# Optimization experiments

Hardware: AMD Instinct MI355X
Metric: run time of the kernel (lower is better)

## Reference

```python
import jax, jax.numpy as jnp
import numpy as np
import math

B, L, D, P = 2, 2048, 256, 32
PI = math.pi


def _layernorm(x, g, b, eps=1e-5):
    m = x.mean(-1, keepdims=True)
    v = x.var(-1, keepdims=True)
    return (x - m) / jnp.sqrt(v + eps) * g + b


def setup_inputs() -> dict:
    key = jax.random.key(0)
    ks = jax.random.split(key, 16)
    sd = 1.0 / math.sqrt(D)
    f32 = jnp.float32
    inp = {
        "x": jax.random.normal(ks[0], (B, L, D), f32),
        # key_encoder: Linear(D, P)
        "key_W": jax.random.normal(ks[1], (D, P), f32) * sd,
        "key_b": jnp.zeros((P,), f32),
        # value_encoder: Linear(D, D)
        "val_W": jax.random.normal(ks[2], (D, D), f32) * sd,
        "val_b": jnp.zeros((D,), f32),
        # refiner: LayerNorm(D), Linear(D, 2D), GELU, Linear(2D, D)
        "ln1_g": jnp.ones((D,), f32),
        "ln1_b": jnp.zeros((D,), f32),
        "W1": jax.random.normal(ks[3], (D, 2 * D), f32) * sd,
        "b1": jnp.zeros((2 * D,), f32),
        "W2": jax.random.normal(ks[4], (2 * D, D), f32) * (1.0 / math.sqrt(2 * D)),
        "b2": jnp.zeros((D,), f32),
        # to_out: LayerNorm(D), Linear(D, D)
        "ln2_g": jnp.ones((D,), f32),
        "ln2_b": jnp.zeros((D,), f32),
        "Wo": jax.random.normal(ks[5], (D, D), f32) * sd,
        "bo": jnp.zeros((D,), f32),
    }
    return inp


def reference(x, key_W, key_b, val_W, val_b, ln1_g, ln1_b, W1, b1, W2, b2,
              ln2_g, ln2_b, Wo, bo):
    # key phases in (-pi, pi); phasor exp(i*theta) handled as (cos, sin)
    phases = jnp.tanh(x @ key_W + key_b) * PI          # (B, L, P)
    values = x @ val_W + val_b                          # (B, L, D)

    cos_p = jnp.cos(phases)
    sin_p = jnp.sin(phases)
    # torch.roll(shifts=1, dims=1) then zero the first position -> shift right, row 0 = 0
    zrow = jnp.zeros_like(cos_p[:, :1])
    cos_s = jnp.concatenate([zrow, cos_p[:, :-1]], axis=1)
    sin_s = jnp.concatenate([zrow, sin_p[:, :-1]], axis=1)

    # odd positions hold values
    vmask = (jnp.arange(L) % 2 == 1).astype(x.dtype)    # (L,)
    mv = values * vmask[None, :, None]                  # (B, L, D)

    # bind: outer product phasor (P) x value (D); real/imag parts
    bound_re = cos_s[..., None] * mv[:, :, None, :]     # (B, L, P, D)
    bound_im = sin_s[..., None] * mv[:, :, None, :]
    mem_re = jnp.cumsum(bound_re, axis=1)
    mem_im = jnp.cumsum(bound_im, axis=1)

    # retrieve: Re[ memory * exp(-i*theta) ] summed over phases
    retrieved = (jnp.einsum('blpd,blp->bld', mem_re, cos_p)
                 + jnp.einsum('blpd,blp->bld', mem_im, sin_p))

    valid = jnp.maximum(jnp.cumsum(vmask), 1.0)         # (L,)
    retrieved = retrieved / (jnp.sqrt(valid)[None, :, None] * math.sqrt(P))

    h = _layernorm(retrieved, ln1_g, ln1_b)
    h = jax.nn.gelu(h @ W1 + b1, approximate=False)
    refined = h @ W2 + b2
    out = x + (_layernorm(refined, ln2_g, ln2_b) @ Wo + bo)
    return out
```

## Files before the change

### kernel.cpp

```cpp
#include <hip/hip_runtime.h>
#include <math.h>

#define BB 2
#define LL 2048
#define DD 256
#define PP 32
#define NC 64
#define PI_F 3.14159265358979323846f

typedef __attribute__((ext_vector_type(8))) short bf16x8;
typedef __attribute__((ext_vector_type(4))) float f32x4;
typedef unsigned short ushort_t;
typedef unsigned int uint_t;

__device__ inline ushort_t f2bf(float x) {
    uint_t u = __float_as_uint(x);
    uint_t r = (u + 0x7fffu + ((u >> 16) & 1u)) >> 16;
    return (ushort_t)r;
}

__global__ __launch_bounds__(256) void prep_key_kernel(
    const float* __restrict__ W1, const float* __restrict__ W2,
    const float* __restrict__ Wo, const float* __restrict__ valW,
    const float* __restrict__ x, const float* __restrict__ key_W,
    const float* __restrict__ key_b,
    ushort_t* __restrict__ W1t, ushort_t* __restrict__ W2t,
    ushort_t* __restrict__ Wot, ushort_t* __restrict__ valWt,
    float2* __restrict__ ph)
{
    const int bid = blockIdx.x;
    const int t = threadIdx.x;
    if (bid < 96) {
        __shared__ float T[64][65];
        const float* W; ushort_t* Wt; int K, N, tile;
        if (bid < 32)      { W = W1;   Wt = W1t;   K = 256; N = 512; tile = bid; }
        else if (bid < 64) { W = W2;   Wt = W2t;   K = 512; N = 256; tile = bid - 32; }
        else if (bid < 80) { W = Wo;   Wt = Wot;   K = 256; N = 256; tile = bid - 64; }
        else               { W = valW; Wt = valWt; K = 256; N = 256; tile = bid - 80; }
        const int ntiles = N / 64;
        const int k0 = (tile / ntiles) * 64, n0 = (tile % ntiles) * 64;
        {
            const int rr = t >> 2, cb = (t & 3) * 16;
            #pragma unroll
            for (int i = 0; i < 16; i += 4) {
                const float4 v = *(const float4*)&W[(k0 + rr) * N + n0 + cb + i];
                T[rr][cb + i + 0] = v.x; T[rr][cb + i + 1] = v.y;
                T[rr][cb + i + 2] = v.z; T[rr][cb + i + 3] = v.w;
            }
        }
        __syncthreads();
        {
            const int n = t >> 2, kb = (t & 3) * 16;
            #pragma unroll
            for (int i = 0; i < 16; ++i)
                Wt[(n0 + n) * K + k0 + kb + i] = f2bf(T[kb + i][n]);
        }
    } else {
        __shared__ ushort_t xt[16][264];
        __shared__ ushort_t kwT[32][264];
        __shared__ float rbuf[4][2][16][17];
        const int row0 = (bid - 96) * 16;
        {
            const int l = t >> 4, cb = (t & 15) * 16;
            const float* src = &x[(long)(row0 + l) * DD + cb];
            ushort_t tmp[16];
            #pragma unroll
            for (int i = 0; i < 4; ++i) {
                const float4 v = *(const float4*)&src[i * 4];
                tmp[i*4+0] = f2bf(v.x); tmp[i*4+1] = f2bf(v.y);
                tmp[i*4+2] = f2bf(v.z); tmp[i*4+3] = f2bf(v.w);
            }
            *(uint4*)&xt[l][cb]     = *(uint4*)&tmp[0];
            *(uint4*)&xt[l][cb + 8] = *(uint4*)&tmp[8];
        }
        {
            #pragma unroll
            for (int i = 0; i < 8; ++i) {
                const int idx4 = i * 256 + t;
                const int k = idx4 >> 3, pc = (idx4 & 7) * 4;
                const float4 v = *(const float4*)&key_W[k * 32 + pc];
                kwT[pc + 0][k] = f2bf(v.x);
                kwT[pc + 1][k] = f2bf(v.y);
                kwT[pc + 2][k] = f2bf(v.z);
                kwT[pc + 3][k] = f2bf(v.w);
            }
        }
        __syncthreads();
        const int wv = t >> 6, lane = t & 63;
        const int qd = lane >> 4, mc = lane & 15;
        f32x4 acc0 = {0.f,0.f,0.f,0.f}, acc1 = {0.f,0.f,0.f,0.f};
        #pragma unroll
        for (int ks = 0; ks < 2; ++ks) {
            const int ko = wv * 64 + ks * 32 + qd * 8;
            const bf16x8 a  = *(const bf16x8*)&xt[mc][ko];
            const bf16x8 b0 = *(const bf16x8*)&kwT[mc][ko];
            const bf16x8 b1 = *(const bf16x8*)&kwT[16 + mc][ko];
            acc0 = __builtin_amdgcn_mfma_f32_16x16x32_bf16(a, b0, acc0, 0, 0, 0);
            acc1 = __builtin_amdgcn_mfma_f32_16x16x32_bf16(a, b1, acc1, 0, 0, 0);
        }
        #pragma unroll
        for (int r = 0; r < 4; ++r) {
            rbuf[wv][0][qd * 4 + r][mc] = acc0[r];
            rbuf[wv][1][qd * 4 + r][mc] = acc1[r];
        }
        __syncthreads();
        #pragma unroll
        for (int rep = 0; rep < 2; ++rep) {
            const int idx = rep * 256 + t;
            const int p = idx & 31, l = idx >> 5;
            const int nf = p >> 4, mcol = p & 15;
            float a = key_b[p] + rbuf[0][nf][l][mcol] + rbuf[1][nf][l][mcol]
                    + rbuf[2][nf][l][mcol] + rbuf[3][nf][l][mcol];
            a = tanhf(a) * PI_F;
            float sn, cs;
            sincosf(a, &sn, &cs);
            ph[(long)(row0 + l) * PP + p] = make_float2(cs, sn);
        }
    }
}

__global__ __launch_bounds__(256) void valbind_kernel(
    const float* __restrict__ x, const float2* __restrict__ ph,
    const ushort_t* __restrict__ valWt, const float* __restrict__ val_b,
    ushort_t* __restrict__ VoddT, float* __restrict__ Mt)
{
    __shared__ ushort_t xsb[16][264];
    __shared__ ushort_t VdT[64][40];
    __shared__ ushort_t phsT[64][40];
    __shared__ float    Ms[64][68];

    const int tid = threadIdx.x;
    const int bid = blockIdx.x;
    const int b  = bid >> 8;
    const int c  = (bid >> 2) & 63;
    const int dq = bid & 3;
    const int base = b * LL;
    const int r0 = 32 * c;

    {
        const int j = tid >> 4, cb = (tid & 15) * 16;
        const float* src = &x[(long)(base + r0 + 2 * j + 1) * DD + cb];
        ushort_t tmp[16];
        #pragma unroll
        for (int i = 0; i < 4; ++i) {
            const float4 v = *(const float4*)&src[i * 4];
            tmp[i*4+0] = f2bf(v.x); tmp[i*4+1] = f2bf(v.y);
            tmp[i*4+2] = f2bf(v.z); tmp[i*4+3] = f2bf(v.w);
        }
        *(uint4*)&xsb[j][cb]     = *(uint4*)&tmp[0];
        *(uint4*)&xsb[j][cb + 8] = *(uint4*)&tmp[8];
    }
    {
        const int j = tid >> 4, qb = (tid & 15) * 4;
        const float4 v = *(const float4*)((const float*)ph +
                              (long)(base + r0 + 2 * j) * 64 + qb);
        phsT[qb + 0][j] = f2bf(v.x);
        phsT[qb + 1][j] = f2bf(v.y);
        phsT[qb + 2][j] = f2bf(v.z);
        phsT[qb + 3][j] = f2bf(v.w);
    }
    for (int e = tid; e < 64 * 16; e += 256) {
        phsT[e >> 4][16 + (e & 15)] = 0;
        VdT[e >> 4][16 + (e & 15)] = 0;
    }
    __syncthreads();

    const int wv = tid >> 6, lane = tid & 63;
    const int qd = lane >> 4, mc = lane & 15;

    f32x4 va = {0.f,0.f,0.f,0.f};
    const int dloc = wv * 16 + mc;
    const int ng = dq * 64 + dloc;
    const ushort_t* B0 = &valWt[(long)ng * 256];
    #pragma unroll
    for (int ks = 0; ks < 8; ++ks) {
        const bf16x8 a  = *(const bf16x8*)&xsb[mc][ks * 32 + qd * 8];
        const bf16x8 b0 = *(const bf16x8*)&B0[ks * 32 + qd * 8];
        va = __builtin_amdgcn_mfma_f32_16x16x32_bf16(a, b0, va, 0, 0, 0);
    }
    {
        const float bb = val_b[ng];
        #pragma unroll
        for (int r = 0; r < 4; ++r)
            VdT[dloc][qd * 4 + r] = f2bf(va[r] + bb);
    }
    __syncthreads();

    const bf16x8 a2 = *(const bf16x8*)&phsT[wv * 16 + mc][qd * 8];
    f32x4 macc[4];
    #pragma unroll
    for (int nf = 0; nf < 4; ++nf) {
        f32x4 z = {0.f,0.f,0.f,0.f};
        const bf16x8 b2 = *(const bf16x8*)&VdT[nf * 16 + mc][qd * 8];
        macc[nf] = __builtin_amdgcn_mfma_f32_16x16x32_bf16(a2, b2, z, 0, 0, 0);
    }
    #pragma unroll
    for (int nf = 0; nf < 4; ++nf) {
        #pragma unroll
        for (int r = 0; r < 4; ++r)
            Ms[nf * 16 + mc][wv * 16 + qd * 4 + r] = macc[nf][r];
    }
    __syncthreads();

    {
        float* dst = &Mt[((long)(b * NC + c) * 256 + dq * 64) * 64];
        #pragma unroll
        for (int p = 0; p < 4; ++p) {
            const int idx4 = p * 256 + tid;
            const int dl = idx4 >> 4, q4 = (idx4 & 15) * 4;
            *(float4*)&dst[dl * 64 + q4] = *(const float4*)&Ms[dl][q4];
        }
    }
    if (tid < 64) {
        ushort_t* vd = &VoddT[((long)(b * NC + c) * 256 + dq * 64 + tid) * 16];
        *(uint4*)&vd[0] = *(const uint4*)&VdT[tid][0];
        *(uint4*)&vd[8] = *(const uint4*)&VdT[tid][8];
    }
}

__global__ __launch_bounds__(256) void prefix_kernel(
    const float* __restrict__ M, ushort_t* __restrict__ Mpre_b)
{
    __shared__ float segsum[4][64];
    const int tid = threadIdx.x;
    const int b  = blockIdx.x >> 8;
    const int cg = blockIdx.x & 255;
    const int col = cg * 64 + (tid & 63);
    const int seg = tid >> 6;
    const long base = (long)b * NC * 16384 + col;

    float v[16], s = 0.f;
    #pragma unroll
    for (int i = 0; i < 16; ++i) {
        v[i] = M[base + (long)(seg * 16 + i) * 16384];
        s += v[i];
    }
    segsum[seg][tid & 63] = s;
    __syncthreads();
    float run = 0.f;
    #pragma unroll
    for (int sg = 0; sg < 3; ++sg)
        if (sg < seg) run += segsum[sg][tid & 63];
    #pragma unroll
    for (int i = 0; i < 16; ++i) {
        const long a = base + (long)(seg * 16 + i) * 16384;
        Mpre_b[a] = f2bf(run);
        run += v[i];
    }
}

__global__ __launch_bounds__(256) void retrieve_kernel(
    const float* __restrict__ ph, const ushort_t* __restrict__ Mpre_b,
    const ushort_t* __restrict__ VoddT,
    const float* __restrict__ ln1_g, const float* __restrict__ ln1_b,
    ushort_t* __restrict__ rhat)
{
    __shared__ ushort_t Bs_m[256][72];
    __shared__ ushort_t Bs_v[256][32];
    __shared__ ushort_t As_ph[16][72];
    __shared__ ushort_t Bs_sh[16][72];
    __shared__ ushort_t As_p[16][32];
    __shared__ float    ref[16][264];

    const int tid = threadIdx.x;
    const int b = blockIdx.x >> 7;
    const int c = (blockIdx.x >> 1) & 63;
    const int h = blockIdx.x & 1;
    const int l0g = 32 * c + 16 * h;
    const long rowbase = (long)b * LL + l0g;

    {
        const ushort_t* src = &Mpre_b[(long)(b * NC + c) * 16384];
        #pragma unroll
        for (int p = 0; p < 8; ++p) {
            const int idx8 = p * 256 + tid;
            const int d = idx8 >> 3, q8 = (idx8 & 7) * 8;
            *(uint4*)&Bs_m[d][q8] = *(const uint4*)&src[idx8 * 8];
        }
    }
    {
        const int r = tid >> 4, q4 = (tid & 15) * 4;
        const float4 v = *(const float4*)&ph[(rowbase + r) * 64 + q4];
        ushort_t t0[4] = {f2bf(v.x), f2bf(v.y), f2bf(v.z), f2bf(v.w)};
        *(uint2*)&As_ph[r][q4] = *(uint2*)t0;
        const float4 w = *(const float4*)&ph[((long)b * LL + 32 * c + 2 * r) * 64 + q4];
        ushort_t t1[4] = {f2bf(w.x), f2bf(w.y), f2bf(w.z), f2bf(w.w)};
        *(uint2*)&Bs_sh[r][q4] = *(uint2*)t1;
    }
    {
        const ushort_t* src = &VoddT[(long)(b * NC + c) * 4096];
        const int j0 = (tid & 1) * 8;
        *(uint4*)&Bs_v[tid >> 1][j0] = *(const uint4*)&src[tid * 8];
        *(uint4*)&Bs_v[(tid + 256) >> 1][j0] = *(const uint4*)&src[(tid + 256) * 8];
        *(uint4*)&Bs_v[tid][16] = make_uint4(0, 0, 0, 0);
        *(uint4*)&Bs_v[tid][24] = make_uint4(0, 0, 0, 0);
        As_p[tid >> 4][16 + (tid & 15)] = 0;
    }
    __syncthreads();

    const int wv = tid >> 6, lane = tid & 63;
    const int qd = lane >> 4, mc = lane & 15;

    {
        f32x4 sacc = {0.f, 0.f, 0.f, 0.f};
        #pragma unroll
        for (int ks = 0; ks < 2; ++ks) {
            const bf16x8 a  = *(const bf16x8*)&As_ph[mc][ks * 32 + qd * 8];
            const bf16x8 bb = *(const bf16x8*)&Bs_sh[mc][ks * 32 + qd * 8];
            sacc = __builtin_amdgcn_mfma_f32_16x16x32_bf16(a, bb, sacc, 0, 0, 0);
        }
        if (wv == 0) {
            #pragma unroll
            for (int r = 0; r < 4; ++r) {
                const int l = qd * 4 + r;
                As_p[l][mc] = (2 * mc + 1 <= 16 * h + l) ? f2bf(sacc[r])
                                                         : (ushort_t)0;
            }
        }
    }

    f32x4 acc[4];
    #pragma unroll
    for (int i = 0; i < 4; ++i) acc[i] = (f32x4){0.f, 0.f, 0.f, 0.f};
    #pragma unroll
    for (int i = 0; i < 4; ++i) {
        const int d0 = wv * 64 + i * 16;
        #pragma unroll
        for (int ks = 0; ks < 2; ++ks) {
            const bf16x8 a  = *(const bf16x8*)&As_ph[mc][ks * 32 + qd * 8];
            const bf16x8 bb = *(const bf16x8*)&Bs_m[d0 + mc][ks * 32 + qd * 8];
            acc[i] = __builtin_amdgcn_mfma_f32_16x16x32_bf16(a, bb, acc[i], 0, 0, 0);
        }
    }
    __syncthreads();

    {
        const bf16x8 a2 = *(const bf16x8*)&As_p[mc][qd * 8];
        #pragma unroll
        for (int i = 0; i < 4; ++i) {
            const int d0 = wv * 64 + i * 16;
            const bf16x8 b2 = *(const bf16x8*)&Bs_v[d0 + mc][qd * 8];
            acc[i] = __builtin_amdgcn_mfma_f32_16x16x32_bf16(a2, b2, acc[i], 0, 0, 0);
        }
    }

    #pragma unroll
    for (int r = 0; r < 4; ++r) {
        const int l = qd * 4 + r;
        int va = (l0g + l + 1) >> 1; if (va < 1) va = 1;
        const float sc = 0.17677669529663687f * rsqrtf((float)va);
        #pragma unroll
        for (int i = 0; i < 4; ++i)
            ref[l][wv * 64 + i * 16 + mc] = acc[i][r] * sc;
    }
    __syncthreads();

    {
        const int row = tid >> 4, cg = (tid & 15) * 16;
        float s = 0.f, sq = 0.f;
        #pragma unroll
        for (int i = 0; i < 16; ++i) {
            const float v = ref[row][cg + i];
            s += v; sq += v * v;
        }
        s += __shfl_xor(s, 1, 16);  sq += __shfl_xor(sq, 1, 16);
        s += __shfl_xor(s, 2, 16);  sq += __shfl_xor(sq, 2, 16);
        s += __shfl_xor(s, 4, 16);  sq += __shfl_xor(sq, 4, 16);
        s += __shfl_xor(s, 8, 16);  sq += __shfl_xor(sq, 8, 16);
        const float m = s * (1.f / 256.f);
        const float inv = rsqrtf(sq * (1.f / 256.f) - m * m + 1e-5f);
        ushort_t o16[16];
        #pragma unroll
        for (int i = 0; i < 16; ++i) {
            const int cc = cg + i;
            o16[i] = f2bf((ref[row][cc] - m) * inv * ln1_g[cc] + ln1_b[cc]);
        }
        ushort_t* dst = &rhat[(rowbase + row) * DD + cg];
        *(uint4*)&dst[0] = *(uint4*)&o16[0];
        *(uint4*)&dst[8] = *(uint4*)&o16[8];
    }
}

__global__ __launch_bounds__(256) void gemm1_kernel(
    const ushort_t* __restrict__ A, const ushort_t* __restrict__ Bt,
    const float* __restrict__ bias, ushort_t* __restrict__ out)
{
    __shared__ ushort_t As[32][136];
    __shared__ ushort_t Bs[64][136];
    const int tid = threadIdx.x;
    const int mt = blockIdx.x & 127;
    const int nt = blockIdx.x >> 7;
    const int m0 = mt * 32, n0 = nt * 64;
    const int wv = tid >> 6, lane = tid & 63;
    const int qd = lane >> 4, mc = lane & 15;

    f32x4 acc0 = {0.f, 0.f, 0.f, 0.f};
    f32x4 acc1 = {0.f, 0.f, 0.f, 0.f};

    const int ar = tid >> 3, ak = (tid & 7) * 16;
    const int bn = tid >> 2, bk = (tid & 3) * 32;

    for (int k0 = 0; k0 < 256; k0 += 128) {
        __syncthreads();
        {
            const ushort_t* sa = &A[(long)(m0 + ar) * 256 + k0 + ak];
            *(uint4*)&As[ar][ak]     = *(const uint4*)&sa[0];
            *(uint4*)&As[ar][ak + 8] = *(const uint4*)&sa[8];
        }
        {
            const ushort_t* src = &Bt[(long)(n0 + bn) * 256 + k0 + bk];
            *(uint4*)&Bs[bn][bk +  0] = *(const uint4*)&src[0];
            *(uint4*)&Bs[bn][bk +  8] = *(const uint4*)&src[8];
            *(uint4*)&Bs[bn][bk + 16] = *(const uint4*)&src[16];
            *(uint4*)&Bs[bn][bk + 24] = *(const uint4*)&src[24];
        }
        __syncthreads();
        #pragma unroll
        for (int ko = 0; ko < 128; ko += 32) {
            const bf16x8 a0 = *(const bf16x8*)&As[mc][ko + qd * 8];
            const bf16x8 a1 = *(const bf16x8*)&As[16 + mc][ko + qd * 8];
            const bf16x8 b  = *(const bf16x8*)&Bs[wv * 16 + mc][ko + qd * 8];
            acc0 = __builtin_amdgcn_mfma_f32_16x16x32_bf16(a0, b, acc0, 0, 0, 0);
            acc1 = __builtin_amdgcn_mfma_f32_16x16x32_bf16(a1, b, acc1, 0, 0, 0);
        }
    }

    const int nn = n0 + wv * 16 + mc;
    const float bb = bias[nn];
    #pragma unroll
    for (int r = 0; r < 4; ++r) {
        const long row0w = m0 + qd * 4 + r;
        float v0 = acc0[r] + bb;
        float v1 = acc1[r] + bb;
        v0 = 0.5f * v0 * (1.f + erff(v0 * 0.70710678118654752f));
        v1 = 0.5f * v1 * (1.f + erff(v1 * 0.70710678118654752f));
        out[row0w * 512 + nn] = f2bf(v0);
        out[(row0w + 16) * 512 + nn] = f2bf(v1);
    }
}

__global__ __launch_bounds__(256) void gemm23_kernel(
    const ushort_t* __restrict__ h, const ushort_t* __restrict__ W2t,
    const float* __restrict__ b2, const float* __restrict__ ln2_g,
    const float* __restrict__ ln2_b, const ushort_t* __restrict__ Wot,
    const float* __restrict__ bo, const float* __restrict__ x,
    float* __restrict__ out)
{
    __shared__ ushort_t As[16][72];
    __shared__ ushort_t Bs[256][72];
    __shared__ float Ct[16][264];
    __shared__ ushort_t shT[16][264];

    const int tid = threadIdx.x;
    const int m0 = blockIdx.x * 16;
    const int wv = tid >> 6, lane = tid & 63;
    const int qd = lane >> 4, mc = lane & 15;

    f32x4 acc[4];
    #pragma unroll
    for (int nf = 0; nf < 4; ++nf) acc[nf] = (f32x4){0.f,0.f,0.f,0.f};

    const int sr = tid >> 3, sk = (tid & 7) * 8;

    for (int k0 = 0; k0 < 512; k0 += 64) {
        __syncthreads();
        if (tid < 128)
            *(uint4*)&As[sr][sk] = *(const uint4*)&h[(long)(m0 + sr) * 512 + k0 + sk];
        #pragma unroll
        for (int rr = 0; rr < 8; ++rr) {
            const int n = rr * 32 + (tid >> 3);
            *(uint4*)&Bs[n][sk] = *(const uint4*)&W2t[(long)n * 512 + k0 + sk];
        }
        __syncthreads();
        #pragma unroll
        for (int ks = 0; ks < 2; ++ks) {
            const bf16x8 a = *(const bf16x8*)&As[mc][ks * 32 + qd * 8];
            #pragma unroll
            for (int nf = 0; nf < 4; ++nf) {
                const bf16x8 b = *(const bf16x8*)&Bs[wv * 64 + nf * 16 + mc][ks * 32 + qd * 8];
                acc[nf] = __builtin_amdgcn_mfma_f32_16x16x32_bf16(a, b, acc[nf], 0, 0, 0);
            }
        }
    }

    #pragma unroll
    for (int nf = 0; nf < 4; ++nf) {
        const int n = wv * 64 + nf * 16 + mc;
        const float bb = b2[n];
        #pragma unroll
        for (int r = 0; r < 4; ++r)
            Ct[qd * 4 + r][n] = acc[nf][r] + bb;
    }
    __syncthreads();

    {
        const int row = tid >> 4, cg = (tid & 15) * 16;
        float s = 0.f, sq = 0.f;
        #pragma unroll
        for (int i = 0; i < 16; ++i) {
            const float v = Ct[row][cg + i];
            s += v; sq += v * v;
        }
        s  += __shfl_xor(s, 1, 16);  sq += __shfl_xor(sq, 1, 16);
        s  += __shfl_xor(s, 2, 16);  sq += __shfl_xor(sq, 2, 16);
        s  += __shfl_xor(s, 4, 16);  sq += __shfl_xor(sq, 4, 16);
        s  += __shfl_xor(s, 8, 16);  sq += __shfl_xor(sq, 8, 16);
        const float m = s * (1.f / 256.f);
        const float inv = rsqrtf(sq * (1.f / 256.f) - m * m + 1e-5f);
        #pragma unroll
        for (int i = 0; i < 16; ++i) {
            const int cc = cg + i;
            shT[row][cc] = f2bf((Ct[row][cc] - m) * inv * ln2_g[cc] + ln2_b[cc]);
        }
    }

    f32x4 acc2[4];
    #pragma unroll
    for (int nf = 0; nf < 4; ++nf) acc2[nf] = (f32x4){0.f,0.f,0.f,0.f};

    for (int k0 = 0; k0 < 256; k0 += 64) {
        __syncthreads();
        #pragma unroll
        for (int rr = 0; rr < 8; ++rr) {
            const int n = rr * 32 + (tid >> 3);
            *(uint4*)&Bs[n][sk] = *(const uint4*)&Wot[(long)n * 256 + k0 + sk];
        }
        __syncthreads();
        #pragma unroll
        for (int ks = 0; ks < 2; ++ks) {
            const bf16x8 a = *(const bf16x8*)&shT[mc][k0 + ks * 32 + qd * 8];
            #pragma unroll
            for (int nf = 0; nf < 4; ++nf) {
                const bf16x8 b = *(const bf16x8*)&Bs[wv * 64 + nf * 16 + mc][ks * 32 + qd * 8];
                acc2[nf] = __builtin_amdgcn_mfma_f32_16x16x32_bf16(a, b, acc2[nf], 0, 0, 0);
            }
        }
    }

    #pragma unroll
    for (int nf = 0; nf < 4; ++nf) {
        const int n = wv * 64 + nf * 16 + mc;
        const float bb = bo[n];
        #pragma unroll
        for (int r = 0; r < 4; ++r) {
            const long row = m0 + qd * 4 + r;
            out[row * DD + n] = acc2[nf][r] + bb + x[row * DD + n];
        }
    }
}

extern "C" void kernel_launch(void* const* d_in, const int* in_sizes, int n_in,
                              void* d_out, int out_size, void* d_ws, size_t ws_size,
                              hipStream_t stream)
{
    const float* x     = (const float*)d_in[0];
    const float* key_W = (const float*)d_in[1];
    const float* key_b = (const float*)d_in[2];
    const float* val_W = (const float*)d_in[3];
    const float* val_b = (const float*)d_in[4];
    const float* ln1_g = (const float*)d_in[5];
    const float* ln1_b = (const float*)d_in[6];
    const float* W1    = (const float*)d_in[7];
    const float* b1    = (const float*)d_in[8];
    const float* W2    = (const float*)d_in[9];
    const float* b2    = (const float*)d_in[10];
    const float* ln2_g = (const float*)d_in[11];
    const float* ln2_b = (const float*)d_in[12];
    const float* Wo    = (const float*)d_in[13];
    const float* bo    = (const float*)d_in[14];
    float* outp = (float*)d_out;

    float* ws = (float*)d_ws;
    float*  ph      = ws;
    float*  Mt      = ws + 262144;
    ushort_t* Mpre_b = (ushort_t*)(Mt + 2097152);
    ushort_t* VoddT  = Mpre_b + 2097152;
    ushort_t* rhat_b = VoddT + 524288;
    ushort_t* W1t   = rhat_b + 1048576;
    ushort_t* W2t   = W1t + 131072;
    ushort_t* Wot   = W2t + 131072;
    ushort_t* valWt = Wot + 65536;
    ushort_t* h_b    = (ushort_t*)Mt;

    prep_key_kernel<<<352, 256, 0, stream>>>(W1, W2, Wo, val_W, x, key_W, key_b,
                                             W1t, W2t, Wot, valWt, (float2*)ph);
    valbind_kernel<<<512, 256, 0, stream>>>(x, (const float2*)ph, valWt, val_b,
                                            VoddT, Mt);
    prefix_kernel<<<512, 256, 0, stream>>>(Mt, Mpre_b);
    retrieve_kernel<<<256, 256, 0, stream>>>(ph, Mpre_b, VoddT, ln1_g, ln1_b, rhat_b);
    gemm1_kernel<<<1024, 256, 0, stream>>>(rhat_b, W1t, b1, h_b);
    gemm23_kernel<<<256, 256, 0, stream>>>(h_b, W2t, b2, ln2_g, ln2_b,
                                           Wot, bo, x, outp);
}
```

Before: 123.5 us.

## Fuse retrieve, MLP GEMMs and output projection into one kernel

```diff
diff --git a/kernel.cpp b/kernel.cpp
--- a/kernel.cpp
+++ b/kernel.cpp
@@ -249,18 +249,25 @@
     }
 }
 
-__global__ __launch_bounds__(256) void retrieve_kernel(
+__global__ __launch_bounds__(256) void retrieve_mlp_kernel(
     const float* __restrict__ ph, const ushort_t* __restrict__ Mpre_b,
     const ushort_t* __restrict__ VoddT,
     const float* __restrict__ ln1_g, const float* __restrict__ ln1_b,
-    ushort_t* __restrict__ rhat)
+    const ushort_t* __restrict__ W1t, const float* __restrict__ b1,
+    const ushort_t* __restrict__ W2t, const float* __restrict__ b2,
+    const float* __restrict__ ln2_g, const float* __restrict__ ln2_b,
+    const ushort_t* __restrict__ Wot, const float* __restrict__ bo,
+    const float* __restrict__ x, float* __restrict__ out)
 {
     __shared__ ushort_t Bs_m[256][72];
     __shared__ ushort_t Bs_v[256][32];
     __shared__ ushort_t As_ph[16][72];
     __shared__ ushort_t Bs_sh[16][72];
     __shared__ ushort_t As_p[16][32];
-    __shared__ float    ref[16][264];
+    __shared__ float    refct[16][264];
+    __shared__ ushort_t rhat_s[16][264];
+    __shared__ ushort_t h_s[16][520];
+    __shared__ ushort_t shT[16][264];
 
     const int tid = threadIdx.x;
     const int b = blockIdx.x >> 7;
@@ -300,6 +307,7 @@
 
     const int wv = tid >> 6, lane = tid & 63;
     const int qd = lane >> 4, mc = lane & 15;
+    const int sk = (tid & 7) * 8;
 
     {
         f32x4 sacc = {0.f, 0.f, 0.f, 0.f};
@@ -351,7 +359,7 @@
         const float sc = 0.17677669529663687f * rsqrtf((float)va);
         #pragma unroll
         for (int i = 0; i < 4; ++i)
-            ref[l][wv * 64 + i * 16 + mc] = acc[i][r] * sc;
+            refct[l][wv * 64 + i * 16 + mc] = acc[i][r] * sc;
     }
     __syncthreads();
 
@@ -360,7 +368,7 @@
         float s = 0.f, sq = 0.f;
         #pragma unroll
         for (int i = 0; i < 16; ++i) {
-            const float v = ref[row][cg + i];
+            const float v = refct[row][cg + i];
             s += v; sq += v * v;
         }
         s += __shfl_xor(s, 1, 16);  sq += __shfl_xor(sq, 1, 16);
@@ -373,123 +381,77 @@
         #pragma unroll
         for (int i = 0; i < 16; ++i) {
             const int cc = cg + i;
-            o16[i] = f2bf((ref[row][cc] - m) * inv * ln1_g[cc] + ln1_b[cc]);
-        }
-        ushort_t* dst = &rhat[(rowbase + row) * DD + cg];
-        *(uint4*)&dst[0] = *(uint4*)&o16[0];
-        *(uint4*)&dst[8] = *(uint4*)&o16[8];
-    }
-}
-
-__global__ __launch_bounds__(256) void gemm1_kernel(
-    const ushort_t* __restrict__ A, const ushort_t* __restrict__ Bt,
-    const float* __restrict__ bias, ushort_t* __restrict__ out)
-{
-    __shared__ ushort_t As[32][136];
-    __shared__ ushort_t Bs[64][136];
-    const int tid = threadIdx.x;
-    const int mt = blockIdx.x & 127;
-    const int nt = blockIdx.x >> 7;
-    const int m0 = mt * 32, n0 = nt * 64;
-    const int wv = tid >> 6, lane = tid & 63;
-    const int qd = lane >> 4, mc = lane & 15;
-
-    f32x4 acc0 = {0.f, 0.f, 0.f, 0.f};
-    f32x4 acc1 = {0.f, 0.f, 0.f, 0.f};
-
-    const int ar = tid >> 3, ak = (tid & 7) * 16;
-    const int bn = tid >> 2, bk = (tid & 3) * 32;
-
-    for (int k0 = 0; k0 < 256; k0 += 128) {
-        __syncthreads();
-        {
-            const ushort_t* sa = &A[(long)(m0 + ar) * 256 + k0 + ak];
-            *(uint4*)&As[ar][ak]     = *(const uint4*)&sa[0];
-            *(uint4*)&As[ar][ak + 8] = *(const uint4*)&sa[8];
-        }
-        {
-            const ushort_t* src = &Bt[(long)(n0 + bn) * 256 + k0 + bk];
-            *(uint4*)&Bs[bn][bk +  0] = *(const uint4*)&src[0];
-            *(uint4*)&Bs[bn][bk +  8] = *(const uint4*)&src[8];
-            *(uint4*)&Bs[bn][bk + 16] = *(const uint4*)&src[16];
-            *(uint4*)&Bs[bn][bk + 24] = *(const uint4*)&src[24];
-        }
-        __syncthreads();
-        #pragma unroll
-        for (int ko = 0; ko < 128; ko += 32) {
-            const bf16x8 a0 = *(const bf16x8*)&As[mc][ko + qd * 8];
-            const bf16x8 a1 = *(const bf16x8*)&As[16 + mc][ko + qd * 8];
-            const bf16x8 b  = *(const bf16x8*)&Bs[wv * 16 + mc][ko + qd * 8];
-            acc0 = __builtin_amdgcn_mfma_f32_16x16x32_bf16(a0, b, acc0, 0, 0, 0);
-            acc1 = __builtin_amdgcn_mfma_f32_16x16x32_bf16(a1, b, acc1, 0, 0, 0);
-        }
-    }
-
-    const int nn = n0 + wv * 16 + mc;
-    const float bb = bias[nn];
-    #pragma unroll
-    for (int r = 0; r < 4; ++r) {
-        const long row0w = m0 + qd * 4 + r;
-        float v0 = acc0[r] + bb;
-        float v1 = acc1[r] + bb;
-        v0 = 0.5f * v0 * (1.f + erff(v0 * 0.70710678118654752f));
-        v1 = 0.5f * v1 * (1.f + erff(v1 * 0.70710678118654752f));
-        out[row0w * 512 + nn] = f2bf(v0);
-        out[(row0w + 16) * 512 + nn] = f2bf(v1);
-    }
-}
-
-__global__ __launch_bounds__(256) void gemm23_kernel(
-    const ushort_t* __restrict__ h, const ushort_t* __restrict__ W2t,
-    const float* __restrict__ b2, const float* __restrict__ ln2_g,
-    const float* __restrict__ ln2_b, const ushort_t* __restrict__ Wot,
-    const float* __restrict__ bo, const float* __restrict__ x,
-    float* __restrict__ out)
-{
-    __shared__ ushort_t As[16][72];
-    __shared__ ushort_t Bs[256][72];
-    __shared__ float Ct[16][264];
-    __shared__ ushort_t shT[16][264];
-
-    const int tid = threadIdx.x;
-    const int m0 = blockIdx.x * 16;
-    const int wv = tid >> 6, lane = tid & 63;
-    const int qd = lane >> 4, mc = lane & 15;
-
-    f32x4 acc[4];
-    #pragma unroll
-    for (int nf = 0; nf < 4; ++nf) acc[nf] = (f32x4){0.f,0.f,0.f,0.f};
-
-    const int sr = tid >> 3, sk = (tid & 7) * 8;
-
+            o16[i] = f2bf((refct[row][cc] - m) * inv * ln1_g[cc] + ln1_b[cc]);
+        }
+        *(uint4*)&rhat_s[row][cg]     = *(uint4*)&o16[0];
+        *(uint4*)&rhat_s[row][cg + 8] = *(uint4*)&o16[8];
+    }
+
+    #pragma unroll
+    for (int nh = 0; nh < 2; ++nh) {
+        f32x4 acc1[4];
+        #pragma unroll
+        for (int nf = 0; nf < 4; ++nf) acc1[nf] = (f32x4){0.f,0.f,0.f,0.f};
+        for (int k0 = 0; k0 < 256; k0 += 64) {
+            __syncthreads();
+            #pragma unroll
+            for (int rr = 0; rr < 8; ++rr) {
+                const int n = rr * 32 + (tid >> 3);
+                *(uint4*)&Bs_m[n][sk] =
+                    *(const uint4*)&W1t[(long)(nh * 256 + n) * 256 + k0 + sk];
+            }
+            __syncthreads();
+            #pragma unroll
+            for (int ks = 0; ks < 2; ++ks) {
+                const bf16x8 a = *(const bf16x8*)&rhat_s[mc][k0 + ks * 32 + qd * 8];
+                #pragma unroll
+                for (int nf = 0; nf < 4; ++nf) {
+                    const bf16x8 bb = *(const bf16x8*)&Bs_m[wv * 64 + nf * 16 + mc][ks * 32 + qd * 8];
+                    acc1[nf] = __builtin_amdgcn_mfma_f32_16x16x32_bf16(a, bb, acc1[nf], 0, 0, 0);
+                }
+            }
+        }
+        #pragma unroll
+        for (int nf = 0; nf < 4; ++nf) {
+            const int n = nh * 256 + wv * 64 + nf * 16 + mc;
+            const float bb = b1[n];
+            #pragma unroll
+            for (int r = 0; r < 4; ++r) {
+                float v = acc1[nf][r] + bb;
+                v = 0.5f * v * (1.f + erff(v * 0.70710678118654752f));
+                h_s[qd * 4 + r][n] = f2bf(v);
+            }
+        }
+    }
+
+    f32x4 acc2[4];
+    #pragma unroll
+    for (int nf = 0; nf < 4; ++nf) acc2[nf] = (f32x4){0.f,0.f,0.f,0.f};
     for (int k0 = 0; k0 < 512; k0 += 64) {
         __syncthreads();
-        if (tid < 128)
-            *(uint4*)&As[sr][sk] = *(const uint4*)&h[(long)(m0 + sr) * 512 + k0 + sk];
         #pragma unroll
         for (int rr = 0; rr < 8; ++rr) {
             const int n = rr * 32 + (tid >> 3);
-            *(uint4*)&Bs[n][sk] = *(const uint4*)&W2t[(long)n * 512 + k0 + sk];
+            *(uint4*)&Bs_m[n][sk] = *(const uint4*)&W2t[(long)n * 512 + k0 + sk];
         }
         __syncthreads();
         #pragma unroll
         for (int ks = 0; ks < 2; ++ks) {
-            const bf16x8 a = *(const bf16x8*)&As[mc][ks * 32 + qd * 8];
+            const bf16x8 a = *(const bf16x8*)&h_s[mc][k0 + ks * 32 + qd * 8];
             #pragma unroll
             for (int nf = 0; nf < 4; ++nf) {
-                const bf16x8 b = *(const bf16x8*)&Bs[wv * 64 + nf * 16 + mc][ks * 32 + qd * 8];
-                acc[nf] = __builtin_amdgcn_mfma_f32_16x16x32_bf16(a, b, acc[nf], 0, 0, 0);
-            }
-        }
-    }
-
+                const bf16x8 bb = *(const bf16x8*)&Bs_m[wv * 64 + nf * 16 + mc][ks * 32 + qd * 8];
+                acc2[nf] = __builtin_amdgcn_mfma_f32_16x16x32_bf16(a, bb, acc2[nf], 0, 0, 0);
+            }
+        }
+    }
     #pragma unroll
     for (int nf = 0; nf < 4; ++nf) {
         const int n = wv * 64 + nf * 16 + mc;
         const float bb = b2[n];
         #pragma unroll
         for (int r = 0; r < 4; ++r)
-            Ct[qd * 4 + r][n] = acc[nf][r] + bb;
+            refct[qd * 4 + r][n] = acc2[nf][r] + bb;
     }
     __syncthreads();
 
@@ -498,7 +460,7 @@
         float s = 0.f, sq = 0.f;
         #pragma unroll
         for (int i = 0; i < 16; ++i) {
-            const float v = Ct[row][cg + i];
+            const float v = refct[row][cg + i];
             s += v; sq += v * v;
         }
         s  += __shfl_xor(s, 1, 16);  sq += __shfl_xor(sq, 1, 16);
@@ -510,20 +472,19 @@
         #pragma unroll
         for (int i = 0; i < 16; ++i) {
             const int cc = cg + i;
-            shT[row][cc] = f2bf((Ct[row][cc] - m) * inv * ln2_g[cc] + ln2_b[cc]);
-        }
-    }
-
-    f32x4 acc2[4];
-    #pragma unroll
-    for (int nf = 0; nf < 4; ++nf) acc2[nf] = (f32x4){0.f,0.f,0.f,0.f};
-
+            shT[row][cc] = f2bf((refct[row][cc] - m) * inv * ln2_g[cc] + ln2_b[cc]);
+        }
+    }
+
+    f32x4 acc3[4];
+    #pragma unroll
+    for (int nf = 0; nf < 4; ++nf) acc3[nf] = (f32x4){0.f,0.f,0.f,0.f};
     for (int k0 = 0; k0 < 256; k0 += 64) {
         __syncthreads();
         #pragma unroll
         for (int rr = 0; rr < 8; ++rr) {
             const int n = rr * 32 + (tid >> 3);
-            *(uint4*)&Bs[n][sk] = *(const uint4*)&Wot[(long)n * 256 + k0 + sk];
+            *(uint4*)&Bs_m[n][sk] = *(const uint4*)&Wot[(long)n * 256 + k0 + sk];
         }
         __syncthreads();
         #pragma unroll
@@ -531,20 +492,19 @@
             const bf16x8 a = *(const bf16x8*)&shT[mc][k0 + ks * 32 + qd * 8];
             #pragma unroll
             for (int nf = 0; nf < 4; ++nf) {
-                const bf16x8 b = *(const bf16x8*)&Bs[wv * 64 + nf * 16 + mc][ks * 32 + qd * 8];
-                acc2[nf] = __builtin_amdgcn_mfma_f32_16x16x32_bf16(a, b, acc2[nf], 0, 0, 0);
-            }
-        }
-    }
-
+                const bf16x8 bb = *(const bf16x8*)&Bs_m[wv * 64 + nf * 16 + mc][ks * 32 + qd * 8];
+                acc3[nf] = __builtin_amdgcn_mfma_f32_16x16x32_bf16(a, bb, acc3[nf], 0, 0, 0);
+            }
+        }
+    }
     #pragma unroll
     for (int nf = 0; nf < 4; ++nf) {
         const int n = wv * 64 + nf * 16 + mc;
         const float bb = bo[n];
         #pragma unroll
         for (int r = 0; r < 4; ++r) {
-            const long row = m0 + qd * 4 + r;
-            out[row * DD + n] = acc2[nf][r] + bb + x[row * DD + n];
+            const long row = rowbase + qd * 4 + r;
+            out[row * DD + n] = acc3[nf][r] + bb + x[row * DD + n];
         }
     }
 }
@@ -580,15 +540,13 @@
     ushort_t* W2t   = W1t + 131072;
     ushort_t* Wot   = W2t + 131072;
     ushort_t* valWt = Wot + 65536;
-    ushort_t* h_b    = (ushort_t*)Mt;
 
     prep_key_kernel<<<352, 256, 0, stream>>>(W1, W2, Wo, val_W, x, key_W, key_b,
                                              W1t, W2t, Wot, valWt, (float2*)ph);
     valbind_kernel<<<512, 256, 0, stream>>>(x, (const float2*)ph, valWt, val_b,
                                             VoddT, Mt);
     prefix_kernel<<<512, 256, 0, stream>>>(Mt, Mpre_b);
-    retrieve_kernel<<<256, 256, 0, stream>>>(ph, Mpre_b, VoddT, ln1_g, ln1_b, rhat_b);
-    gemm1_kernel<<<1024, 256, 0, stream>>>(rhat_b, W1t, b1, h_b);
-    gemm23_kernel<<<256, 256, 0, stream>>>(h_b, W2t, b2, ln2_g, ln2_b,
-                                           Wot, bo, x, outp);
+    retrieve_mlp_kernel<<<256, 256, 0, stream>>>(ph, Mpre_b, VoddT, ln1_g, ln1_b,
+                                                 W1t, b1, W2t, b2, ln2_g, ln2_b,
+                                                 Wot, bo, x, outp);
 }
```

Result: slower. 126.5 us (+2.4%).
